# Kernel optimization log

Measured on AMD Instinct MI355X. Metric: run time of the kernel, lower is better.

The kernel has to match this reference:

```python
import jax, jax.numpy as jnp
import numpy as np

N_CLS = 4
NUM_QUERIES = 256
TEMPERATURE = 0.07
NEG_INF = -1e9


def setup_inputs() -> dict:
    key = jax.random.key(0)
    k1, k2, k3, k4, k5, k6 = jax.random.split(key, 6)
    B, C, H, W = 8, 512, 64, 64
    K = 3072
    pred_s = jax.random.normal(k1, (B, N_CLS, H, W), dtype=jnp.float32)
    feat_s_raw = jax.random.normal(k2, (B, C, H, W), dtype=jnp.float32)
    feat_t_raw = jax.random.normal(k3, (B, C, H, W), dtype=jnp.float32)
    target = jax.random.randint(k4, (B, H, W), 0, N_CLS, dtype=jnp.int64)
    queue = jax.random.normal(k5, (C, K), dtype=jnp.float32)
    queue = queue / jnp.linalg.norm(queue, axis=0, keepdims=True)  # F.normalize(queue, dim=0)
    queue_labels = jax.random.randint(k6, (1, K), 0, N_CLS, dtype=jnp.int64)
    return {"pred_s": pred_s, "feat_s_raw": feat_s_raw, "feat_t_raw": feat_t_raw,
            "target": target, "queue": queue, "queue_labels": queue_labels}


def _l2norm(x, axis):
    return x / jnp.clip(jnp.linalg.norm(x, axis=axis, keepdims=True), 1e-12)


def reference(pred_s, feat_s_raw, feat_t_raw, target, queue, queue_labels):
    # softmax over class dim (probs are only consumed in the hard (random=False)
    # branch of find_hard_sampling; module default is random=True)
    probs_s = jax.nn.softmax(pred_s, axis=1)
    fs = _l2norm(feat_s_raw, axis=1)   # [B, C, H, W]
    ft = _l2norm(feat_t_raw, axis=1)
    B, C, H, W = fs.shape

    # permute(0,2,3,1).flatten(0,2) -> [N, C], matching target.reshape(-1)
    rep = jnp.transpose(fs, (0, 2, 3, 1)).reshape(-1, C)
    rep_t = jnp.transpose(ft, (0, 2, 3, 1)).reshape(-1, C)
    tflat = target.reshape(-1)  # [N]

    # find_hard_sampling, random=True path: for each segment, draw NUM_QUERIES
    # indices uniformly from that segment's valid pixels (assumes every class
    # is present, which holds w.h.p. at this resolution).
    key = jax.random.key(42)
    keys = jax.random.split(key, N_CLS + 1)

    def sample_class(k, cls):
        logits = jnp.where(tflat == cls, 0.0, NEG_INF)  # uniform over valid pixels
        return jax.random.categorical(k, logits, shape=(NUM_QUERIES,))

    idx = jax.vmap(sample_class)(keys[:N_CLS], jnp.arange(N_CLS)).reshape(-1)  # [N_CLS*NQ]
    labels = jnp.repeat(jnp.arange(N_CLS), NUM_QUERIES)

    # shuffle (get_shuffle_ids)
    perm = jax.random.permutation(keys[N_CLS], idx.shape[0])
    idx = idx[perm]
    labels = labels[perm]

    feats_s = rep[idx]     # [n, C] random gather (memory-bound)
    feats_t = rep_t[idx]

    l_pos = jnp.einsum('nc,nc->n', feats_s, feats_t)[:, None]   # [n, 1]
    l_neg = jnp.einsum('nc,ck->nk', feats_s, queue)             # [n, K]
    logits = jnp.concatenate([l_pos, l_neg], axis=1) / TEMPERATURE

    # non-targeted mask: eq(labels_cur, queue_labels)
    mask = (labels[:, None] == queue_labels[0][None, :]).astype(logits.dtype)
    return logits, mask, labels
```

## Files before the change

### kernel.cpp

```cpp
#include <hip/hip_runtime.h>
#include <stdint.h>

#define N_PIX   32768
#define C_DIM   512
#define K_Q     3072
#define NCLS    4
#define NQ      256
#define N_SAMP  1024
#define HW      4096
#define L_ROW   3073
#define KH      1024
#define KP      1536

typedef float f32x4 __attribute__((ext_vector_type(4)));
typedef short s16x8 __attribute__((ext_vector_type(8)));

__device__ inline unsigned short f2bf(float f) {
  uint32_t u = __float_as_uint(f);
  return (unsigned short)((u + 0x7FFFu + ((u >> 16) & 1u)) >> 16);
}
__device__ inline float bf2f(unsigned short h) {
  return __uint_as_float(((uint32_t)h) << 16);
}

__host__ __device__ inline void tf2x32(uint32_t k0, uint32_t k1,
                                       uint32_t x0, uint32_t x1,
                                       uint32_t& o0, uint32_t& o1) {
  uint32_t ks2 = k0 ^ k1 ^ 0x1BD11BDAu;
  x0 += k0; x1 += k1;
#define ROTL_(v,d) (((v)<<(d))|((v)>>(32-(d))))
#define RND_(r) { x0 += x1; x1 = ROTL_(x1, r); x1 ^= x0; }
  RND_(13) RND_(15) RND_(26) RND_(6)
  x0 += k1; x1 += ks2 + 1u;
  RND_(17) RND_(29) RND_(16) RND_(24)
  x0 += ks2; x1 += k0 + 2u;
  RND_(13) RND_(15) RND_(26) RND_(6)
  x0 += k0; x1 += k1 + 3u;
  RND_(17) RND_(29) RND_(16) RND_(24)
  x0 += k1; x1 += ks2 + 4u;
  RND_(13) RND_(15) RND_(26) RND_(6)
  x0 += ks2; x1 += k0 + 5u;
  o0 = x0; o1 = x1;
#undef RND_
#undef ROTL_
}

__global__ void k_zero(int* cnt) {
  if (threadIdx.x < NCLS) cnt[threadIdx.x] = 0;
}

__global__ __launch_bounds__(256) void k_compact(const int* __restrict__ target,
                                                 int* __restrict__ cnt,
                                                 int* __restrict__ lists) {
  __shared__ int lcnt[NCLS];
  __shared__ int lbase[NCLS];
  int tid = threadIdx.x;
  if (tid < NCLS) lcnt[tid] = 0;
  __syncthreads();
  int p = blockIdx.x * 256 + tid;
  int c = target[p];
  int lpos = atomicAdd(&lcnt[c], 1);
  __syncthreads();
  if (tid < NCLS) lbase[tid] = atomicAdd(&cnt[tid], lcnt[tid]);
  __syncthreads();
  lists[c * N_PIX + lbase[c] + lpos] = p;
}

__global__ __launch_bounds__(256) void k_sample(
    const int* __restrict__ cnt, const int* __restrict__ lists,
    int* __restrict__ samp,
    uint32_t k0a, uint32_t k0b, uint32_t k1a, uint32_t k1b,
    uint32_t k2a, uint32_t k2b, uint32_t k3a, uint32_t k3b) {
  int c = blockIdx.y;
  int q = blockIdx.x;
  uint32_t ka, kb;
  if      (c == 0) { ka = k0a; kb = k0b; }
  else if (c == 1) { ka = k1a; kb = k1b; }
  else if (c == 2) { ka = k2a; kb = k2b; }
  else             { ka = k3a; kb = k3b; }

  int nv = cnt[c];
  const int* lst = lists + c * N_PIX;
  unsigned long long best = 0ull;
  for (int t = threadIdx.x; t < nv; t += 256) {
    int p = lst[t];
    uint32_t j = (uint32_t)(q * N_PIX + p);
    uint32_t o0, o1;
    tf2x32(ka, kb, 0u, j, o0, o1);
    uint32_t bits = o0 ^ o1;
    unsigned long long v =
        ((unsigned long long)(bits >> 9) << 15) | (unsigned)(32767 - p);
    if (v > best) best = v;
  }
  __shared__ unsigned long long red[256];
  red[threadIdx.x] = best;
  __syncthreads();
  for (int s = 128; s > 0; s >>= 1) {
    if (threadIdx.x < s && red[threadIdx.x + s] > red[threadIdx.x])
      red[threadIdx.x] = red[threadIdx.x + s];
    __syncthreads();
  }
  if (threadIdx.x == 0)
    samp[c * NQ + q] = 32767 - (int)(red[0] & 0x7FFFull);
}

__global__ __launch_bounds__(64) void k_perm(
    const int* __restrict__ samp, int* __restrict__ idx_final,
    int* __restrict__ labels_shuf, float* __restrict__ out_labels,
    uint32_t sk0, uint32_t sk1) {
  __shared__ uint32_t keys_s[N_SAMP];
  int lt = threadIdx.x;
  for (int t = lt; t < N_SAMP; t += 64) {
    uint32_t o0, o1;
    tf2x32(sk0, sk1, 0u, (uint32_t)t, o0, o1);
    keys_s[t] = o0 ^ o1;
  }
  __syncthreads();
  int i = blockIdx.x * 64 + lt;
  uint32_t ki = keys_s[i];
  int rank = 0;
#pragma unroll 4
  for (int j = 0; j < N_SAMP; ++j) {
    uint32_t kj = keys_s[j];
    rank += (int)((kj < ki) | ((kj == ki) & (j < i)));
  }
  idx_final[rank] = samp[i];
  int lab = i >> 8;
  labels_shuf[rank] = lab;
  out_labels[rank] = (float)lab;
}

__global__ __launch_bounds__(256) void k_gather(
    const float* __restrict__ fs, const float* __restrict__ ft,
    const int* __restrict__ idx_final, unsigned short* __restrict__ A2,
    float* __restrict__ out_logits) {
  int n = blockIdx.x;
  int p = idx_final[n];
  int b = p >> 12;
  int hw = p & (HW - 1);
  const float* fsb = fs + (size_t)b * C_DIM * HW + hw;
  const float* ftb = ft + (size_t)b * C_DIM * HW + hw;
  int c0 = threadIdx.x, c1 = threadIdx.x + 256;
  float s0 = fsb[(size_t)c0 * HW], s1 = fsb[(size_t)c1 * HW];
  float t0 = ftb[(size_t)c0 * HW], t1 = ftb[(size_t)c1 * HW];

  __shared__ float red[256];
  __shared__ float ns_sh, nt_sh;

  red[threadIdx.x] = s0 * s0 + s1 * s1;
  __syncthreads();
  for (int s = 128; s > 0; s >>= 1) {
    if (threadIdx.x < s) red[threadIdx.x] += red[threadIdx.x + s];
    __syncthreads();
  }
  if (threadIdx.x == 0) ns_sh = fmaxf(sqrtf(red[0]), 1e-12f);
  __syncthreads();

  red[threadIdx.x] = t0 * t0 + t1 * t1;
  __syncthreads();
  for (int s = 128; s > 0; s >>= 1) {
    if (threadIdx.x < s) red[threadIdx.x] += red[threadIdx.x + s];
    __syncthreads();
  }
  if (threadIdx.x == 0) nt_sh = fmaxf(sqrtf(red[0]), 1e-12f);
  __syncthreads();

  float ns = ns_sh, nt = nt_sh;
  float a0 = s0 / ns, a1 = s1 / ns;
  float b0 = t0 / nt, b1 = t1 / nt;

  unsigned short h0 = f2bf(a0), h1 = f2bf(a1);
  unsigned short l0 = f2bf(a0 - bf2f(h0)), l1 = f2bf(a1 - bf2f(h1));
  unsigned short* row = A2 + (size_t)n * KH;
  row[c0]       = h0;  row[c1]       = h1;
  row[512 + c0] = l0;  row[512 + c1] = l1;

  red[threadIdx.x] = a0 * b0 + a1 * b1;
  __syncthreads();
  for (int s = 128; s > 0; s >>= 1) {
    if (threadIdx.x < s) red[threadIdx.x] += red[threadIdx.x + s];
    __syncthreads();
  }
  if (threadIdx.x == 0)
    out_logits[(size_t)n * L_ROW] = red[0] * (1.0f / 0.07f);
}

__global__ __launch_bounds__(256) void k_convq(const float* __restrict__ queue,
                                               unsigned short* __restrict__ B2) {
  __shared__ float tile[64][65];
  int tid = threadIdx.x;
  int n0 = blockIdx.x * 64;
  int k0 = blockIdx.y * 64;
#pragma unroll
  for (int it = 0; it < 4; ++it) {
    int r = (tid >> 4) + it * 16;
    int c4 = (tid & 15) * 4;
    float4 v = *(const float4*)(queue + (size_t)(k0 + r) * K_Q + n0 + c4);
    tile[r][c4 + 0] = v.x; tile[r][c4 + 1] = v.y;
    tile[r][c4 + 2] = v.z; tile[r][c4 + 3] = v.w;
  }
  __syncthreads();
  int tn = tid >> 2;
  int kc = (tid & 3) * 16;
  unsigned short* rowp = B2 + (size_t)(n0 + tn) * KH + k0 + kc;
#pragma unroll
  for (int g8 = 0; g8 < 2; ++g8) {
    s16x8 vhi, vlo;
#pragma unroll
    for (int j = 0; j < 8; ++j) {
      float v = tile[kc + g8 * 8 + j][tn];
      unsigned short h = f2bf(v);
      vhi[j] = (short)h;
      vlo[j] = (short)f2bf(v - bf2f(h));
    }
    *(s16x8*)(rowp + g8 * 8)       = vhi;
    *(s16x8*)(rowp + 512 + g8 * 8) = vlo;
  }
}

__global__ __launch_bounds__(256) void k_gemm(
    const unsigned short* __restrict__ A2,
    const unsigned short* __restrict__ B2,
    float* __restrict__ out) {
  __shared__ unsigned short sAB[16384];
  int tid  = threadIdx.x;
  int lane = tid & 63;
  int wave = tid >> 6;
  int wm = wave >> 1, wn = wave & 1;
  int bm = blockIdx.x * 128;
  int bn = blockIdx.y * 128;

  int rbase = wave * 32 + (lane >> 3);
  int lcol  = (lane & 7) * 8;

  f32x4 acc[4][4] = {};
  s16x8 ra[4], rb[4];

  const int NSTEP = KP / 64;
  {
#pragma unroll
    for (int c = 0; c < 4; ++c) {
      int r = rbase + c * 8;
      ra[c] = *(const s16x8*)(A2 + (size_t)(bm + r) * KH + lcol);
      rb[c] = *(const s16x8*)(B2 + (size_t)(bn + r) * KH + lcol);
    }
#pragma unroll
    for (int c = 0; c < 4; ++c) {
      int r = rbase + c * 8;
      int slot = ((lane & 7) ^ (r & 7)) * 8;
      *(s16x8*)&sAB[r * 64 + slot]        = ra[c];
      *(s16x8*)&sAB[8192 + r * 64 + slot] = rb[c];
    }
  }
  __syncthreads();

  for (int s = 0; s < NSTEP; ++s) {
    if (s + 1 < NSTEP) {
      int kp = (s + 1) * 64;
      int sA = (kp < 512) ? kp : kp - 512;
      int sB = (kp < 1024) ? kp : kp - 1024;
#pragma unroll
      for (int c = 0; c < 4; ++c) {
        int r = rbase + c * 8;
        ra[c] = *(const s16x8*)(A2 + (size_t)(bm + r) * KH + sA + lcol);
        rb[c] = *(const s16x8*)(B2 + (size_t)(bn + r) * KH + sB + lcol);
      }
    }
#pragma unroll
    for (int kk = 0; kk < 2; ++kk) {
      int g = kk * 4 + (lane >> 4);
      s16x8 af[4], bfr[4];
#pragma unroll
      for (int mi = 0; mi < 4; ++mi) {
        int rowL = wm * 64 + mi * 16 + (lane & 15);
        af[mi] = *(s16x8*)&sAB[rowL * 64 + ((g ^ (rowL & 7)) << 3)];
      }
#pragma unroll
      for (int ni = 0; ni < 4; ++ni) {
        int rowN = wn * 64 + ni * 16 + (lane & 15);
        bfr[ni] = *(s16x8*)&sAB[8192 + rowN * 64 + ((g ^ (rowN & 7)) << 3)];
      }
#pragma unroll
      for (int mi = 0; mi < 4; ++mi)
#pragma unroll
        for (int ni = 0; ni < 4; ++ni)
          acc[mi][ni] = __builtin_amdgcn_mfma_f32_16x16x32_bf16(
              af[mi], bfr[ni], acc[mi][ni], 0, 0, 0);
    }
    __syncthreads();
    if (s + 1 < NSTEP) {
#pragma unroll
      for (int c = 0; c < 4; ++c) {
        int r = rbase + c * 8;
        int slot = ((lane & 7) ^ (r & 7)) * 8;
        *(s16x8*)&sAB[r * 64 + slot]        = ra[c];
        *(s16x8*)&sAB[8192 + r * 64 + slot] = rb[c];
      }
      __syncthreads();
    }
  }

  const float sc = 1.0f / 0.07f;
#pragma unroll
  for (int mi = 0; mi < 4; ++mi) {
#pragma unroll
    for (int ni = 0; ni < 4; ++ni) {
#pragma unroll
      for (int j = 0; j < 4; ++j) {
        int rl = wm * 64 + mi * 16 + ((lane >> 4) << 2) + j;
        int cl = wn * 64 + ni * 16 + (lane & 15);
        out[(size_t)(bm + rl) * L_ROW + 1 + (bn + cl)] = acc[mi][ni][j] * sc;
      }
    }
  }
}

__global__ __launch_bounds__(256) void k_mask(const int* __restrict__ labels,
                                              const int* __restrict__ qlab,
                                              float* __restrict__ mask) {
  int row = blockIdx.x;
  int lab = labels[row];
  float* mrow = mask + (size_t)row * K_Q;
#pragma unroll
  for (int j = 0; j < 12; ++j) {
    int col = j * 256 + threadIdx.x;
    mrow[col] = (lab == qlab[col]) ? 1.0f : 0.0f;
  }
}

extern "C" void kernel_launch(void* const* d_in, const int* in_sizes, int n_in,
                              void* d_out, int out_size, void* d_ws, size_t ws_size,
                              hipStream_t stream) {
  const float* fs     = (const float*)d_in[1];
  const float* ft     = (const float*)d_in[2];
  const int*   target = (const int*)d_in[3];
  const float* queue  = (const float*)d_in[4];
  const int*   qlab   = (const int*)d_in[5];
  float* out = (float*)d_out;

  char* ws = (char*)d_ws;
  int* cnt   = (int*)(ws + 0);
  int* samp  = (int*)(ws + 4096);
  int* idxf  = (int*)(ws + 8192);
  int* labs  = (int*)(ws + 12288);
  int* lists = (int*)(ws + 16384);

  float* maskBase = out + (size_t)N_SAMP * L_ROW;
  unsigned short* B2 = (unsigned short*)maskBase;
  unsigned short* A2 = (unsigned short*)maskBase + (size_t)K_Q * KH;

  uint32_t ck[5][2];
  for (int i = 0; i < 5; ++i)
    tf2x32(0u, 42u, 0u, (uint32_t)i, ck[i][0], ck[i][1]);
  uint32_t sk0, sk1;
  tf2x32(ck[4][0], ck[4][1], 0u, 1u, sk0, sk1);

  float* out_labels = out + (size_t)N_SAMP * L_ROW + (size_t)N_SAMP * K_Q;

  k_zero<<<1, 64, 0, stream>>>(cnt);
  k_compact<<<N_PIX / 256, 256, 0, stream>>>(target, cnt, lists);
  k_convq<<<dim3(K_Q / 64, C_DIM / 64), 256, 0, stream>>>(queue, B2);
  k_sample<<<dim3(NQ, NCLS), 256, 0, stream>>>(
      cnt, lists, samp,
      ck[0][0], ck[0][1], ck[1][0], ck[1][1],
      ck[2][0], ck[2][1], ck[3][0], ck[3][1]);
  k_perm<<<16, 64, 0, stream>>>(samp, idxf, labs, out_labels, sk0, sk1);
  k_gather<<<N_SAMP, 256, 0, stream>>>(fs, ft, idxf, A2, out);
  k_gemm<<<dim3(N_SAMP / 128, K_Q / 128), 256, 0, stream>>>(A2, B2, out);
  k_mask<<<N_SAMP, 256, 0, stream>>>(labs, qlab, maskBase);
}
```

Measured before the change: 258.7 us.

## Fuse mask into GEMM epilogue, shrink GEMM tiles, merge zeroing into convq

The mask computation is moved into the GEMM epilogue, with labels staged in shared memory, which removes the separate mask kernel. The GEMM tile drops from 128x128 to 64x64, raising the block count from 192 to 768 to fill more CUs. The counter zeroing is folded into k_convq to save a launch. The bf16 split operand buffers move out of the output mask region into the workspace, since the mask is now written concurrently with the GEMM. Smaller tiles lower per-block operand reuse and increase global traffic.

```diff
diff --git a/kernel.cpp b/kernel.cpp
--- a/kernel.cpp
+++ b/kernel.cpp
@@ -45,8 +45,40 @@
 #undef ROTL_
 }
 
-__global__ void k_zero(int* cnt) {
-  if (threadIdx.x < NCLS) cnt[threadIdx.x] = 0;
+__global__ __launch_bounds__(256) void k_convq(const float* __restrict__ queue,
+                                               unsigned short* __restrict__ B2,
+                                               int* __restrict__ cnt) {
+  if (blockIdx.x == 0 && blockIdx.y == 0 && threadIdx.x < NCLS)
+    cnt[threadIdx.x] = 0;
+  __shared__ float tile[64][65];
+  int tid = threadIdx.x;
+  int n0 = blockIdx.x * 64;
+  int k0 = blockIdx.y * 64;
+#pragma unroll
+  for (int it = 0; it < 4; ++it) {
+    int r = (tid >> 4) + it * 16;
+    int c4 = (tid & 15) * 4;
+    float4 v = *(const float4*)(queue + (size_t)(k0 + r) * K_Q + n0 + c4);
+    tile[r][c4 + 0] = v.x; tile[r][c4 + 1] = v.y;
+    tile[r][c4 + 2] = v.z; tile[r][c4 + 3] = v.w;
+  }
+  __syncthreads();
+  int tn = tid >> 2;
+  int kc = (tid & 3) * 16;
+  unsigned short* rowp = B2 + (size_t)(n0 + tn) * KH + k0 + kc;
+#pragma unroll
+  for (int g8 = 0; g8 < 2; ++g8) {
+    s16x8 vhi, vlo;
+#pragma unroll
+    for (int j = 0; j < 8; ++j) {
+      float v = tile[kc + g8 * 8 + j][tn];
+      unsigned short h = f2bf(v);
+      vhi[j] = (short)h;
+      vlo[j] = (short)f2bf(v - bf2f(h));
+    }
+    *(s16x8*)(rowp + g8 * 8)       = vhi;
+    *(s16x8*)(rowp + 512 + g8 * 8) = vlo;
+  }
 }
 
 __global__ __launch_bounds__(256) void k_compact(const int* __restrict__ target,
@@ -185,72 +217,37 @@
     out_logits[(size_t)n * L_ROW] = red[0] * (1.0f / 0.07f);
 }
 
-__global__ __launch_bounds__(256) void k_convq(const float* __restrict__ queue,
-                                               unsigned short* __restrict__ B2) {
-  __shared__ float tile[64][65];
-  int tid = threadIdx.x;
-  int n0 = blockIdx.x * 64;
-  int k0 = blockIdx.y * 64;
-#pragma unroll
-  for (int it = 0; it < 4; ++it) {
-    int r = (tid >> 4) + it * 16;
-    int c4 = (tid & 15) * 4;
-    float4 v = *(const float4*)(queue + (size_t)(k0 + r) * K_Q + n0 + c4);
-    tile[r][c4 + 0] = v.x; tile[r][c4 + 1] = v.y;
-    tile[r][c4 + 2] = v.z; tile[r][c4 + 3] = v.w;
-  }
-  __syncthreads();
-  int tn = tid >> 2;
-  int kc = (tid & 3) * 16;
-  unsigned short* rowp = B2 + (size_t)(n0 + tn) * KH + k0 + kc;
-#pragma unroll
-  for (int g8 = 0; g8 < 2; ++g8) {
-    s16x8 vhi, vlo;
-#pragma unroll
-    for (int j = 0; j < 8; ++j) {
-      float v = tile[kc + g8 * 8 + j][tn];
-      unsigned short h = f2bf(v);
-      vhi[j] = (short)h;
-      vlo[j] = (short)f2bf(v - bf2f(h));
-    }
-    *(s16x8*)(rowp + g8 * 8)       = vhi;
-    *(s16x8*)(rowp + 512 + g8 * 8) = vlo;
-  }
-}
-
 __global__ __launch_bounds__(256) void k_gemm(
     const unsigned short* __restrict__ A2,
     const unsigned short* __restrict__ B2,
+    const int* __restrict__ labels,
+    const int* __restrict__ qlab,
     float* __restrict__ out) {
-  __shared__ unsigned short sAB[16384];
+  __shared__ unsigned short sAB[8192];
   int tid  = threadIdx.x;
   int lane = tid & 63;
   int wave = tid >> 6;
   int wm = wave >> 1, wn = wave & 1;
-  int bm = blockIdx.x * 128;
-  int bn = blockIdx.y * 128;
-
-  int rbase = wave * 32 + (lane >> 3);
-  int lcol  = (lane & 7) * 8;
-
-  f32x4 acc[4][4] = {};
-  s16x8 ra[4], rb[4];
+  int bm = blockIdx.x * 64;
+  int bn = blockIdx.y * 64;
+
+  int r0 = tid >> 3;
+  int g0 = tid & 7;
+  int slot0 = ((g0 ^ (r0 & 7)) << 3);
+
+  f32x4 acc[2][2] = {};
+  s16x8 ra[2], rb[2];
 
   const int NSTEP = KP / 64;
   {
-#pragma unroll
-    for (int c = 0; c < 4; ++c) {
-      int r = rbase + c * 8;
-      ra[c] = *(const s16x8*)(A2 + (size_t)(bm + r) * KH + lcol);
-      rb[c] = *(const s16x8*)(B2 + (size_t)(bn + r) * KH + lcol);
-    }
-#pragma unroll
-    for (int c = 0; c < 4; ++c) {
-      int r = rbase + c * 8;
-      int slot = ((lane & 7) ^ (r & 7)) * 8;
-      *(s16x8*)&sAB[r * 64 + slot]        = ra[c];
-      *(s16x8*)&sAB[8192 + r * 64 + slot] = rb[c];
-    }
+    ra[0] = *(const s16x8*)(A2 + (size_t)(bm + r0)      * KH + g0 * 8);
+    ra[1] = *(const s16x8*)(A2 + (size_t)(bm + r0 + 32) * KH + g0 * 8);
+    rb[0] = *(const s16x8*)(B2 + (size_t)(bn + r0)      * KH + g0 * 8);
+    rb[1] = *(const s16x8*)(B2 + (size_t)(bn + r0 + 32) * KH + g0 * 8);
+    *(s16x8*)&sAB[r0 * 64 + slot0]               = ra[0];
+    *(s16x8*)&sAB[(r0 + 32) * 64 + slot0]        = ra[1];
+    *(s16x8*)&sAB[4096 + r0 * 64 + slot0]        = rb[0];
+    *(s16x8*)&sAB[4096 + (r0 + 32) * 64 + slot0] = rb[1];
   }
   __syncthreads();
 
@@ -259,72 +256,63 @@
       int kp = (s + 1) * 64;
       int sA = (kp < 512) ? kp : kp - 512;
       int sB = (kp < 1024) ? kp : kp - 1024;
-#pragma unroll
-      for (int c = 0; c < 4; ++c) {
-        int r = rbase + c * 8;
-        ra[c] = *(const s16x8*)(A2 + (size_t)(bm + r) * KH + sA + lcol);
-        rb[c] = *(const s16x8*)(B2 + (size_t)(bn + r) * KH + sB + lcol);
-      }
+      ra[0] = *(const s16x8*)(A2 + (size_t)(bm + r0)      * KH + sA + g0 * 8);
+      ra[1] = *(const s16x8*)(A2 + (size_t)(bm + r0 + 32) * KH + sA + g0 * 8);
+      rb[0] = *(const s16x8*)(B2 + (size_t)(bn + r0)      * KH + sB + g0 * 8);
+      rb[1] = *(const s16x8*)(B2 + (size_t)(bn + r0 + 32) * KH + sB + g0 * 8);
     }
 #pragma unroll
     for (int kk = 0; kk < 2; ++kk) {
       int g = kk * 4 + (lane >> 4);
-      s16x8 af[4], bfr[4];
-#pragma unroll
-      for (int mi = 0; mi < 4; ++mi) {
-        int rowL = wm * 64 + mi * 16 + (lane & 15);
+      s16x8 af[2], bfr[2];
+#pragma unroll
+      for (int mi = 0; mi < 2; ++mi) {
+        int rowL = wm * 32 + mi * 16 + (lane & 15);
         af[mi] = *(s16x8*)&sAB[rowL * 64 + ((g ^ (rowL & 7)) << 3)];
       }
 #pragma unroll
-      for (int ni = 0; ni < 4; ++ni) {
-        int rowN = wn * 64 + ni * 16 + (lane & 15);
-        bfr[ni] = *(s16x8*)&sAB[8192 + rowN * 64 + ((g ^ (rowN & 7)) << 3)];
+      for (int ni = 0; ni < 2; ++ni) {
+        int rowN = wn * 32 + ni * 16 + (lane & 15);
+        bfr[ni] = *(s16x8*)&sAB[4096 + rowN * 64 + ((g ^ (rowN & 7)) << 3)];
       }
 #pragma unroll
-      for (int mi = 0; mi < 4; ++mi)
-#pragma unroll
-        for (int ni = 0; ni < 4; ++ni)
+      for (int mi = 0; mi < 2; ++mi)
+#pragma unroll
+        for (int ni = 0; ni < 2; ++ni)
           acc[mi][ni] = __builtin_amdgcn_mfma_f32_16x16x32_bf16(
               af[mi], bfr[ni], acc[mi][ni], 0, 0, 0);
     }
     __syncthreads();
     if (s + 1 < NSTEP) {
-#pragma unroll
-      for (int c = 0; c < 4; ++c) {
-        int r = rbase + c * 8;
-        int slot = ((lane & 7) ^ (r & 7)) * 8;
-        *(s16x8*)&sAB[r * 64 + slot]        = ra[c];
-        *(s16x8*)&sAB[8192 + r * 64 + slot] = rb[c];
+      *(s16x8*)&sAB[r0 * 64 + slot0]               = ra[0];
+      *(s16x8*)&sAB[(r0 + 32) * 64 + slot0]        = ra[1];
+      *(s16x8*)&sAB[4096 + r0 * 64 + slot0]        = rb[0];
+      *(s16x8*)&sAB[4096 + (r0 + 32) * 64 + slot0] = rb[1];
+      __syncthreads();
+    }
+  }
+
+  int* labsh = (int*)sAB;
+  if (tid < 64)            labsh[tid] = labels[bm + tid];
+  else if (tid < 128)      labsh[tid] = qlab[bn + (tid - 64)];
+  __syncthreads();
+
+  float* out_mask = out + (size_t)N_SAMP * L_ROW;
+  const float sc = 1.0f / 0.07f;
+#pragma unroll
+  for (int mi = 0; mi < 2; ++mi) {
+#pragma unroll
+    for (int ni = 0; ni < 2; ++ni) {
+#pragma unroll
+      for (int j = 0; j < 4; ++j) {
+        int rl = wm * 32 + mi * 16 + ((lane >> 4) << 2) + j;
+        int cl = wn * 32 + ni * 16 + (lane & 15);
+        int row = bm + rl, col = bn + cl;
+        out[(size_t)row * L_ROW + 1 + col] = acc[mi][ni][j] * sc;
+        out_mask[(size_t)row * K_Q + col] =
+            (labsh[rl] == labsh[64 + cl]) ? 1.0f : 0.0f;
       }
-      __syncthreads();
-    }
-  }
-
-  const float sc = 1.0f / 0.07f;
-#pragma unroll
-  for (int mi = 0; mi < 4; ++mi) {
-#pragma unroll
-    for (int ni = 0; ni < 4; ++ni) {
-#pragma unroll
-      for (int j = 0; j < 4; ++j) {
-        int rl = wm * 64 + mi * 16 + ((lane >> 4) << 2) + j;
-        int cl = wn * 64 + ni * 16 + (lane & 15);
-        out[(size_t)(bm + rl) * L_ROW + 1 + (bn + cl)] = acc[mi][ni][j] * sc;
-      }
-    }
-  }
-}
-
-__global__ __launch_bounds__(256) void k_mask(const int* __restrict__ labels,
-                                              const int* __restrict__ qlab,
-                                              float* __restrict__ mask) {
-  int row = blockIdx.x;
-  int lab = labels[row];
-  float* mrow = mask + (size_t)row * K_Q;
-#pragma unroll
-  for (int j = 0; j < 12; ++j) {
-    int col = j * 256 + threadIdx.x;
-    mrow[col] = (lab == qlab[col]) ? 1.0f : 0.0f;
+    }
   }
 }
 
@@ -344,10 +332,8 @@
   int* idxf  = (int*)(ws + 8192);
   int* labs  = (int*)(ws + 12288);
   int* lists = (int*)(ws + 16384);
-
-  float* maskBase = out + (size_t)N_SAMP * L_ROW;
-  unsigned short* B2 = (unsigned short*)maskBase;
-  unsigned short* A2 = (unsigned short*)maskBase + (size_t)K_Q * KH;
+  unsigned short* A2 = (unsigned short*)(ws + (1u << 20));
+  unsigned short* B2 = (unsigned short*)(ws + (4u << 20));
 
   uint32_t ck[5][2];
   for (int i = 0; i < 5; ++i)
@@ -357,15 +343,14 @@
 
   float* out_labels = out + (size_t)N_SAMP * L_ROW + (size_t)N_SAMP * K_Q;
 
-  k_zero<<<1, 64, 0, stream>>>(cnt);
+  k_convq<<<dim3(K_Q / 64, C_DIM / 64), 256, 0, stream>>>(queue, B2, cnt);
   k_compact<<<N_PIX / 256, 256, 0, stream>>>(target, cnt, lists);
-  k_convq<<<dim3(K_Q / 64, C_DIM / 64), 256, 0, stream>>>(queue, B2);
   k_sample<<<dim3(NQ, NCLS), 256, 0, stream>>>(
       cnt, lists, samp,
       ck[0][0], ck[0][1], ck[1][0], ck[1][1],
       ck[2][0], ck[2][1], ck[3][0], ck[3][1]);
   k_perm<<<16, 64, 0, stream>>>(samp, idxf, labs, out_labels, sk0, sk1);
   k_gather<<<N_SAMP, 256, 0, stream>>>(fs, ft, idxf, A2, out);
-  k_gemm<<<dim3(N_SAMP / 128, K_Q / 128), 256, 0, stream>>>(A2, B2, out);
-  k_mask<<<N_SAMP, 256, 0, stream>>>(labs, qlab, maskBase);
-}
+  k_gemm<<<dim3(N_SAMP / 64, K_Q / 64), 256, 0, stream>>>(
+      A2, B2, labs, qlab, out);
+}
```

Result: faster. 244.0 us (-5.7%).
